# Kernel optimization log

Measured on AMD Instinct MI355X. Metric: run time of the kernel, lower is better.

Reference implementation:

```python
import jax, jax.numpy as jnp
import numpy as np

B, S, E = 2, 2048, 2048
KV, QPG, HD = 4, 4, 128  # 16 total heads, head_size=128
ROPE_THETA = 10000.0


def _rope_cos_sin(seq_len, head_size, dtype):
    inv_freq = 1.0 / (ROPE_THETA ** (jnp.arange(0, head_size, 2, dtype=jnp.float32) / head_size))
    pos = jnp.arange(seq_len, dtype=jnp.float32)
    freqs = pos[:, None] * inv_freq[None, :]            # [S, HD/2]
    emb = jnp.concatenate([freqs, freqs], axis=-1)       # [S, HD]
    return jnp.cos(emb).astype(dtype), jnp.sin(emb).astype(dtype)


def _rotate_half(x):
    x1, x2 = jnp.split(x, 2, axis=-1)
    return jnp.concatenate([-x2, x1], axis=-1)


def _apply_rope(x, cos, sin):
    # x: [..., S, HD]; cos/sin: [S, HD]
    return x * cos + _rotate_half(x) * sin


def setup_inputs() -> dict:
    key = jax.random.key(0)
    ks = jax.random.split(key, 8)
    scale = 0.02
    return {
        "x": jax.random.normal(ks[0], (B, S, E), jnp.float32),
        "wq": jax.random.normal(ks[1], (KV, QPG, HD, E), jnp.float32) * scale,
        "bq": jax.random.normal(ks[2], (KV, QPG, HD), jnp.float32) * scale,
        "wk": jax.random.normal(ks[3], (KV, HD, E), jnp.float32) * scale,
        "bk": jax.random.normal(ks[4], (KV, HD), jnp.float32) * scale,
        "wv": jax.random.normal(ks[5], (KV, HD, E), jnp.float32) * scale,
        "bv": jax.random.normal(ks[6], (KV, HD), jnp.float32) * scale,
        "wo": jax.random.normal(ks[7], (E, E), jnp.float32) * scale,
    }


def reference(x, wq, bq, wk, bk, wv, bv, wo):
    # QKV projections (out_first linear: y = W x + b)
    q = jnp.einsum('bse,kghe->bkgsh', x, wq) + bq[None, :, :, None, :]   # [B,KV,QPG,S,HD]
    k = jnp.einsum('bse,khe->bksh', x, wk) + bk[None, :, None, :]        # [B,KV,S,HD]
    v = jnp.einsum('bse,khe->bksh', x, wv) + bv[None, :, None, :]        # [B,KV,S,HD]

    cos, sin = _rope_cos_sin(S, HD, x.dtype)
    q = _apply_rope(q, cos, sin)
    k = _apply_rope(k, cos, sin)

    # GQA scaled dot-product attention with causal mask
    scale = 1.0 / jnp.sqrt(jnp.asarray(HD, x.dtype))
    scores = jnp.einsum('bkgsh,bkth->bkgst', q, k) * scale               # [B,KV,QPG,S,S]
    causal = jnp.tril(jnp.ones((S, S), dtype=bool))
    scores = jnp.where(causal, scores, jnp.asarray(-1e9, scores.dtype))
    att = jax.nn.softmax(scores, axis=-1)
    out = jnp.einsum('bkgst,bkth->bkgsh', att, v)                        # [B,KV,QPG,S,HD]

    # flatten (kv_heads, q_heads_per_group, head_size) -> heads*head_size and project
    out = out.transpose(0, 3, 1, 2, 4).reshape(B, S, KV * QPG * HD)      # [B,S,E]
    return jnp.einsum('bsf,ef->bse', out, wo)
```

## Files before the change

### kernel.cpp

```cpp
#include <hip/hip_runtime.h>

typedef unsigned short u16;
typedef short s16x8 __attribute__((ext_vector_type(8)));
typedef float f32x4 __attribute__((ext_vector_type(4)));
typedef float f32x16 __attribute__((ext_vector_type(16)));

__device__ __forceinline__ u16 f2bf(float f) {
  union { float f; unsigned u; } x; x.f = f;
  unsigned r = (x.u + 0x7fffu + ((x.u >> 16) & 1u)) >> 16;
  return (u16)r;
}
__device__ __forceinline__ unsigned bfbits_t(float f) {
  union { float f; unsigned u; } x; x.f = f;
  return x.u >> 16;
}
__device__ __forceinline__ float bf2f(u16 u) {
  union { unsigned u; float f; } x; x.u = ((unsigned)u) << 16;
  return x.f;
}

__device__ __forceinline__ void load_lds16(const u16* g, void* lds) {
  __builtin_amdgcn_global_load_lds(
      (const __attribute__((address_space(1))) unsigned int*)g,
      (__attribute__((address_space(3))) unsigned int*)lds, 16, 0, 0);
}

__global__ __launch_bounds__(256) void prep_kernel(
    const float* __restrict__ x,
    const float* __restrict__ wq, const float* __restrict__ wk,
    const float* __restrict__ wv,
    const float* __restrict__ bq, const float* __restrict__ bk,
    const float* __restrict__ bv,
    const float* __restrict__ wo,
    u16* __restrict__ xb, u16* __restrict__ wqkv,
    float* __restrict__ bqkv, u16* __restrict__ wob,
    float* __restrict__ cosb, float* __restrict__ sinb) {
  const int R0 = 2097152;
  const int R1 = R0 + 1572864;
  const int R2 = R1 + 1048576;
  const int R3 = R2 + 768;
  const int R4 = R3 + 131072;
  for (int id = blockIdx.x * 256 + threadIdx.x; id < R4; id += gridDim.x * 256) {
    if (id < R0) {
      float4 v = ((const float4*)x)[id];
      u16* d = xb + (size_t)id * 4;
      d[0] = f2bf(v.x); d[1] = f2bf(v.y); d[2] = f2bf(v.z); d[3] = f2bf(v.w);
    } else if (id < R1) {
      int g = id - R0;
      int row = g >> 9, c4 = (g & 511) * 4;
      const float* src; int srow;
      if (row < 2048)      { src = wq; srow = row; }
      else if (row < 2560) { src = wk; srow = row - 2048; }
      else                 { src = wv; srow = row - 2560; }
      float4 v = *(const float4*)&src[(size_t)srow * 2048 + c4];
      u16* d = wqkv + (size_t)row * 2048 + c4;
      d[0] = f2bf(v.x); d[1] = f2bf(v.y); d[2] = f2bf(v.z); d[3] = f2bf(v.w);
    } else if (id < R2) {
      int g = id - R1;
      float4 v = ((const float4*)wo)[g];
      u16* d = wob + (size_t)g * 4;
      d[0] = f2bf(v.x); d[1] = f2bf(v.y); d[2] = f2bf(v.z); d[3] = f2bf(v.w);
    } else if (id < R3) {
      int g4 = (id - R2) * 4;
      float4 v;
      if (g4 < 2048)      v = *(const float4*)&bq[g4];
      else if (g4 < 2560) v = *(const float4*)&bk[g4 - 2048];
      else                v = *(const float4*)&bv[g4 - 2560];
      *(float4*)&bqkv[g4] = v;
    } else {
      int g = id - R3;
      int s = g >> 6, i = g & 63;
      float freq = powf(10000.0f, -(float)i / 64.0f);
      float ang = (float)s * freq;
      cosb[g] = cosf(ang);
      sinb[g] = sinf(ang);
    }
  }
}

__global__ __launch_bounds__(256) void rope_all_kernel(u16* __restrict__ Qb,
                                                       u16* __restrict__ Kbuf,
                                                       const float* __restrict__ cosb,
                                                       const float* __restrict__ sinb) {
  const int total = (32 + 8) * 2048 * 64;
  for (int id = blockIdx.x * 256 + threadIdx.x; id < total; id += gridDim.x * 256) {
    int i = id & 63;
    int rs = id >> 6;
    int s = rs & 2047;
    u16* p;
    size_t base;
    if (rs < 65536) { p = Qb;   base = (size_t)rs * 128; }
    else            { p = Kbuf; base = (size_t)(rs - 65536) * 128; }
    float x1 = bf2f(p[base + i]);
    float x2 = bf2f(p[base + i + 64]);
    float c = cosb[s * 64 + i], sn = sinb[s * 64 + i];
    p[base + i]      = f2bf(x1 * c - x2 * sn);
    p[base + i + 64] = f2bf(x2 * c + x1 * sn);
  }
}

__global__ __launch_bounds__(256) void transpose_v_kernel(const u16* __restrict__ V,
                                                          u16* __restrict__ Vt) {
  __shared__ u16 tile[64][130];
  const int t = threadIdx.x;
  const int hb = blockIdx.x, s0 = blockIdx.y * 64;
  const u16* src = V + ((size_t)hb * 2048 + s0) * 128;
#pragma unroll
  for (int i = 0; i < 4; ++i) {
    int c = i * 256 + t;
    int s = c >> 4, d8 = (c & 15) * 8;
    *(s16x8*)&tile[s][d8] = *(const s16x8*)&src[(size_t)s * 128 + d8];
  }
  __syncthreads();
  u16* dst = Vt + (size_t)hb * 128 * 2048 + s0;
#pragma unroll
  for (int i = 0; i < 4; ++i) {
    int c = i * 256 + t;
    int d = c & 127, s8 = (c >> 7) * 8;
    s16x8 v;
#pragma unroll
    for (int e = 0; e < 8; ++e) v[e] = (short)tile[s8 + e][d];
    *(s16x8*)&dst[(size_t)d * 2048 + s8] = v;
  }
}

__global__ __launch_bounds__(512) void gemm_bt_kernel(
    const u16* __restrict__ A, const u16* __restrict__ Bw,
    const float* __restrict__ bias,
    float* __restrict__ C, int ldc,
    u16* __restrict__ Qp, u16* __restrict__ Kp, u16* __restrict__ Vp,
    int M, int N, int K, int mode) {
  __shared__ u16 sA[128 * 64];
  __shared__ u16 sB[128 * 64];
  const int t = threadIdx.x;
  const int w = t >> 6, l = t & 63;
  const int lg = l >> 4, lr = l & 15;
  const int wm = (w >> 2) * 64, wn = (w & 3) * 32;
  const int m0 = blockIdx.y * 128, n0 = blockIdx.x * 128;

  f32x4 acc[4][2];
#pragma unroll
  for (int i = 0; i < 4; ++i)
#pragma unroll
    for (int j = 0; j < 2; ++j)
#pragma unroll
      for (int r = 0; r < 4; ++r) acc[i][j][r] = 0.0f;

  for (int k0 = 0; k0 < K; k0 += 64) {
#pragma unroll
    for (int i = 0; i < 2; ++i) {
      int c = i * 512 + t;
      int row = c >> 3, cc = (c & 7) ^ (row & 7);
      load_lds16(A + (size_t)(m0 + row) * K + k0 + cc * 8,
                 (char*)sA + i * 8192 + w * 1024);
      load_lds16(Bw + (size_t)(n0 + row) * K + k0 + cc * 8,
                 (char*)sB + i * 8192 + w * 1024);
    }
    __syncthreads();
#pragma unroll
    for (int kc = 0; kc < 2; ++kc) {
      const int rch = (((kc * 4 + lg) ^ (lr & 7)) * 8);
      s16x8 af[4], bf[2];
#pragma unroll
      for (int m = 0; m < 4; ++m)
        af[m] = *(const s16x8*)&sA[(wm + m * 16 + lr) * 64 + rch];
#pragma unroll
      for (int n = 0; n < 2; ++n)
        bf[n] = *(const s16x8*)&sB[(wn + n * 16 + lr) * 64 + rch];
#pragma unroll
      for (int m = 0; m < 4; ++m)
#pragma unroll
        for (int n = 0; n < 2; ++n)
          acc[m][n] = __builtin_amdgcn_mfma_f32_16x16x32_bf16(af[m], bf[n], acc[m][n], 0, 0, 0);
    }
    __syncthreads();
  }

#pragma unroll
  for (int m = 0; m < 4; ++m) {
#pragma unroll
    for (int n = 0; n < 2; ++n) {
#pragma unroll
      for (int r = 0; r < 4; ++r) {
        int row = m0 + wm + m * 16 + (lg << 2) + r;
        int col = n0 + wn + n * 16 + lr;
        float val = acc[m][n][r];
        if (mode == 0) {
          val += bias[col];
          int b = row >> 11, s = row & 2047;
          u16 bvv = f2bf(val);
          if (col < 2048) {
            int h = col >> 7, d = col & 127;
            Qp[(((size_t)(b * 16 + h)) * 2048 + s) * 128 + d] = bvv;
          } else if (col < 2560) {
            int cc = col - 2048; int kh = cc >> 7, d = cc & 127;
            Kp[(((size_t)(b * 4 + kh)) * 2048 + s) * 128 + d] = bvv;
          } else {
            int cc = col - 2560; int kh = cc >> 7, d = cc & 127;
            Vp[(((size_t)(b * 4 + kh)) * 2048 + s) * 128 + d] = bvv;
          }
        } else {
          C[(size_t)row * ldc + col] = val;
        }
      }
    }
  }
}

__device__ const int PH_QC[16] = {7,-1, 7,0, 6,-1, 6,1, 5,-1, 5,2, 4,-1, 4,3};
__device__ const int PH_J0[16] = {0, 0, 18,0, 0, 0, 18,0, 0, 0, 18,0, 0, 0, 18,0};
__device__ const int PH_NT[16] = {18,0, 14,4, 18,0, 10,8, 18,0, 6,12, 18,0, 2,16};
__device__ const int PH_MD[16] = {1, 0, 2, 0, 1, 0, 2, 0, 1, 0, 2, 0, 1, 0, 2, 0};

__global__ __launch_bounds__(512) void flash_mfma_kernel(const u16* __restrict__ Q,
                                                         const u16* __restrict__ Kb,
                                                         const u16* __restrict__ Vtb,
                                                         u16* __restrict__ O,
                                                         u16* __restrict__ po,
                                                         float* __restrict__ pml) {
  const int S = 2048;
  __shared__ u16 sK[64 * 128];
  __shared__ u16 sVt[2 * 128 * 64];

  const int t = threadIdx.x, w = t >> 6, l = t & 63;
  const int l31 = l & 31, hi = l >> 5;
  const int bh = blockIdx.x, b = bh >> 4, h = bh & 15, kvh = h >> 2;
  const int slot = blockIdx.y;

  const u16* kbase = Kb + ((size_t)(b * 4 + kvh)) * S * 128;
  const u16* vtbase = Vtb + ((size_t)(b * 4 + kvh)) * 128 * S;

  const float C2 = 0.12753785f;

  auto stageK = [&](int kt) {
#pragma unroll
    for (int i = 0; i < 2; ++i) {
      int c = i * 512 + w * 64 + l;
      int j = c >> 4, cc = (c & 15) ^ (j & 7);
      load_lds16(kbase + ((size_t)(kt * 64 + j) * 128 + cc * 8),
                 (char*)sK + (i * 8192 + w * 1024));
    }
  };
  auto stageV = [&](int kt, int buf) {
#pragma unroll
    for (int i = 0; i < 2; ++i) {
      int c = i * 512 + w * 64 + l;
      int d = c >> 3, cc = (c & 7) ^ (d & 7);
      load_lds16(vtbase + ((size_t)d * S + kt * 64 + cc * 8),
                 (char*)sVt + buf * 16384 + (i * 8192 + w * 1024));
    }
  };

#pragma unroll 1
  for (int ph = 0; ph < 2; ++ph) {
    const int qc = PH_QC[slot * 2 + ph];
    const int ntc = PH_NT[slot * 2 + ph];
    if (ntc == 0) break;
    const int j0 = PH_J0[slot * 2 + ph];
    const int md = PH_MD[slot * 2 + ph];
    const int qw = qc * 256 + w * 32;
    const int q_glob = qw + l31;

    const u16* qbase = Q + ((size_t)bh * S + qw) * 128;
    s16x8 qb[8];
#pragma unroll
    for (int ks = 0; ks < 8; ++ks)
      qb[ks] = *(const s16x8*)&qbase[(size_t)l31 * 128 + ks * 16 + hi * 8];

    f32x16 o0, o1, o2, o3;
#pragma unroll
    for (int r = 0; r < 16; ++r) { o0[r] = 0.f; o1[r] = 0.f; o2[r] = 0.f; o3[r] = 0.f; }
    float mrun = -3e38f, lsum = 0.0f;

    stageV(j0, 0);
    stageK(j0);
    __syncthreads();

    int cur = 0;
    for (int kt2 = 0; kt2 < ntc; ++kt2) {
      const int kt = j0 + kt2;
      const bool act = (kt * 64 <= qw + 31);
      const bool more = (kt2 + 1 < ntc);

      if (more) stageV(kt + 1, cur ^ 1);

      f32x16 sc0, sc1;
      if (act) {
#pragma unroll
        for (int r = 0; r < 16; ++r) { sc0[r] = 0.f; sc1[r] = 0.f; }
        __builtin_amdgcn_s_setprio(1);
#pragma unroll
        for (int ks = 0; ks < 8; ++ks) {
          int chk = (2 * ks + hi) ^ (l31 & 7);
          s16x8 kf0 = *(const s16x8*)&sK[l31 * 128 + chk * 8];
          s16x8 kf1 = *(const s16x8*)&sK[(32 + l31) * 128 + chk * 8];
          sc0 = __builtin_amdgcn_mfma_f32_32x32x16_bf16(kf0, qb[ks], sc0, 0, 0, 0);
          sc1 = __builtin_amdgcn_mfma_f32_32x32x16_bf16(kf1, qb[ks], sc1, 0, 0, 0);
        }
        __builtin_amdgcn_s_setprio(0);
      }

      __syncthreads();

      if (more) stageK(kt + 1);

      if (act) {
        const u16* sVc = &sVt[cur * 8192];

        if (kt * 64 + 63 > qw) {
          const int j0m = kt * 64;
#pragma unroll
          for (int r = 0; r < 16; ++r) {
            int jr = j0m + (r & 3) + 8 * (r >> 2) + 4 * hi;
            sc0[r] = (jr <= q_glob) ? sc0[r] : -3e38f;
            sc1[r] = (jr + 32 <= q_glob) ? sc1[r] : -3e38f;
          }
        }

        float tm[16];
#pragma unroll
        for (int r = 0; r < 16; ++r) tm[r] = fmaxf(sc0[r], sc1[r]);
#pragma unroll
        for (int s2 = 8; s2 >= 1; s2 >>= 1)
#pragma unroll
          for (int r = 0; r < s2; ++r) tm[r] = fmaxf(tm[r], tm[r + s2]);
        float mt = fmaxf(tm[0], __shfl_xor(tm[0], 32));
        float mt2 = mt * C2;
        bool resc = (mt2 > mrun + 8.0f);
        if (resc) {
          float Mn = mt2;
          float corr = exp2f(mrun - Mn);
          lsum *= corr;
#pragma unroll
          for (int r = 0; r < 16; ++r) {
            o0[r] *= corr; o1[r] *= corr; o2[r] *= corr; o3[r] *= corr;
          }
          mrun = Mn;
        }
        const float Mn = mrun;

        unsigned pk[16];
        float lacc = 0.0f;
#pragma unroll
        for (int m = 0; m < 8; ++m) {
          float pa_ = exp2f(__builtin_fmaf(sc0[2 * m], C2, -Mn));
          float pb_ = exp2f(__builtin_fmaf(sc0[2 * m + 1], C2, -Mn));
          lacc += pa_ + pb_;
          pk[m] = (bfbits_t(pb_) << 16) | bfbits_t(pa_);
        }
#pragma unroll
        for (int m = 0; m < 8; ++m) {
          float pa_ = exp2f(__builtin_fmaf(sc1[2 * m], C2, -Mn));
          float pb_ = exp2f(__builtin_fmaf(sc1[2 * m + 1], C2, -Mn));
          lacc += pa_ + pb_;
          pk[8 + m] = (bfbits_t(pb_) << 16) | bfbits_t(pa_);
        }
        lsum += lacc;

        unsigned pkx[16];
#pragma unroll
        for (int i = 0; i < 16; ++i) pkx[i] = __shfl_xor(pk[i], 32);

        __builtin_amdgcn_s_setprio(1);
#pragma unroll
        for (int ks = 0; ks < 4; ++ks) {
          const int base = (ks >> 1) * 8 + 4 * (ks & 1);
          unsigned pw[4];
          pw[0] = hi ? pkx[base + 2] : pk[base + 0];
          pw[1] = hi ? pkx[base + 3] : pk[base + 1];
          pw[2] = hi ? pk[base + 2] : pkx[base + 0];
          pw[3] = hi ? pk[base + 3] : pkx[base + 1];
          s16x8 pa = *(const s16x8*)pw;
#pragma unroll
          for (int dt = 0; dt < 4; ++dt) {
            int d = dt * 32 + l31;
            s16x8 vt = *(const s16x8*)&sVc[d * 64 + (((2 * ks + hi) ^ (d & 7)) * 8)];
            if (dt == 0) o0 = __builtin_amdgcn_mfma_f32_32x32x16_bf16(vt, pa, o0, 0, 0, 0);
            if (dt == 1) o1 = __builtin_amdgcn_mfma_f32_32x32x16_bf16(vt, pa, o1, 0, 0, 0);
            if (dt == 2) o2 = __builtin_amdgcn_mfma_f32_32x32x16_bf16(vt, pa, o2, 0, 0, 0);
            if (dt == 3) o3 = __builtin_amdgcn_mfma_f32_32x32x16_bf16(vt, pa, o3, 0, 0, 0);
          }
        }
        __builtin_amdgcn_s_setprio(0);
      }

      __syncthreads();
      cur ^= 1;
    }

    float ls = lsum + __shfl_xor(lsum, 32);
    float inv = (ls > 0.0f) ? 1.0f / ls : 0.0f;
    if (md == 0) {
      size_t obase = ((size_t)b * S + q_glob) * 2048 + h * 128;
#pragma unroll
      for (int dt = 0; dt < 4; ++dt) {
        const f32x16& ov = (dt == 0) ? o0 : (dt == 1) ? o1 : (dt == 2) ? o2 : o3;
#pragma unroll
        for (int g = 0; g < 4; ++g) {
          int d0 = dt * 32 + 8 * g + 4 * hi;
          unsigned u0 = (unsigned)f2bf(ov[4 * g] * inv) | ((unsigned)f2bf(ov[4 * g + 1] * inv) << 16);
          unsigned u1 = (unsigned)f2bf(ov[4 * g + 2] * inv) | ((unsigned)f2bf(ov[4 * g + 3] * inv) << 16);
          uint2 u; u.x = u0; u.y = u1;
          *(uint2*)&O[obase + d0] = u;
        }
      }
    } else {
      const int pid = ((bh << 2) + (qc - 4)) * 2 + (md - 1);
      const int qrow = w * 32 + l31;
      size_t pbase = (size_t)pid * 32768 + (size_t)qrow * 128;
#pragma unroll
      for (int dt = 0; dt < 4; ++dt) {
        const f32x16& ov = (dt == 0) ? o0 : (dt == 1) ? o1 : (dt == 2) ? o2 : o3;
#pragma unroll
        for (int g = 0; g < 4; ++g) {
          int d0 = dt * 32 + 8 * g + 4 * hi;
          unsigned u0 = (unsigned)f2bf(ov[4 * g] * inv) | ((unsigned)f2bf(ov[4 * g + 1] * inv) << 16);
          unsigned u1 = (unsigned)f2bf(ov[4 * g + 2] * inv) | ((unsigned)f2bf(ov[4 * g + 3] * inv) << 16);
          uint2 u; u.x = u0; u.y = u1;
          *(uint2*)&po[pbase + d0] = u;
        }
      }
      if (hi == 0) {
        pml[pid * 512 + qrow * 2]     = mrun;
        pml[pid * 512 + qrow * 2 + 1] = ls;
      }
    }
    if (ph == 0 && PH_NT[slot * 2 + 1] != 0) __syncthreads();
  }
}

__global__ __launch_bounds__(256) void flash_merge_kernel(const u16* __restrict__ po,
                                                          const float* __restrict__ pml,
                                                          u16* __restrict__ att) {
  const int t = threadIdx.x;
  const int tl = blockIdx.x >> 4;
  const int row = (blockIdx.x & 15) * 16 + (t >> 4);
  const int d8 = (t & 15) * 8;
  const int hh2 = tl >> 2, qc = (tl & 3) + 4;
  const int pid0 = tl * 2, pid1 = pid0 + 1;
  float m0 = pml[pid0 * 512 + row * 2], l0 = pml[pid0 * 512 + row * 2 + 1];
  float m1 = pml[pid1 * 512 + row * 2], l1 = pml[pid1 * 512 + row * 2 + 1];
  float M = fmaxf(m0, m1);
  float w0 = l0 * exp2f(m0 - M), w1 = l1 * exp2f(m1 - M);
  float inv = 1.0f / (w0 + w1);
  w0 *= inv; w1 *= inv;
  s16x8 a = *(const s16x8*)&po[(size_t)pid0 * 32768 + row * 128 + d8];
  s16x8 c = *(const s16x8*)&po[(size_t)pid1 * 32768 + row * 128 + d8];
  int b = hh2 >> 4, hh = hh2 & 15;
  size_t base = ((size_t)b * 2048 + qc * 256 + row) * 2048 + hh * 128 + d8;
  u16 outv[8];
#pragma unroll
  for (int e = 0; e < 8; ++e)
    outv[e] = f2bf(w0 * bf2f((u16)a[e]) + w1 * bf2f((u16)c[e]));
  *(s16x8*)&att[base] = *(const s16x8*)outv;
}


extern "C" void kernel_launch(void* const* d_in, const int* in_sizes, int n_in,
                              void* d_out, int out_size, void* d_ws, size_t ws_size,
                              hipStream_t stream) {
  const float* x  = (const float*)d_in[0];
  const float* wq = (const float*)d_in[1];
  const float* bq = (const float*)d_in[2];
  const float* wk = (const float*)d_in[3];
  const float* bk = (const float*)d_in[4];
  const float* wv = (const float*)d_in[5];
  const float* bv = (const float*)d_in[6];
  const float* wo = (const float*)d_in[7];
  float* out = (float*)d_out;

  char* ws = (char*)d_ws;
  u16* xb    = (u16*)ws;    ws += (size_t)4096 * 2048 * 2;
  u16* wqkv  = (u16*)ws;    ws += (size_t)3072 * 2048 * 2;
  float* bqkv = (float*)ws; ws += (size_t)3072 * 4;
  u16* wob   = (u16*)ws;    ws += (size_t)2048 * 2048 * 2;
  u16* Qb    = (u16*)ws;    ws += (size_t)32 * 2048 * 128 * 2;
  u16* Kbuf  = (u16*)ws;    ws += (size_t)8 * 2048 * 128 * 2;
  u16* Vbuf  = (u16*)ws;    ws += (size_t)8 * 2048 * 128 * 2;
  u16* Vt    = (u16*)ws;    ws += (size_t)8 * 128 * 2048 * 2;
  float* cosb = (float*)ws; ws += (size_t)2048 * 64 * 4;
  float* sinb = (float*)ws; ws += (size_t)2048 * 64 * 4;
  u16* att   = (u16*)ws;    ws += (size_t)4096 * 2048 * 2;

  u16* po = xb;
  float* pml = (float*)Vbuf;

  prep_kernel<<<2048, 256, 0, stream>>>(x, wq, wk, wv, bq, bk, bv, wo,
                                        xb, wqkv, bqkv, wob, cosb, sinb);

  gemm_bt_kernel<<<dim3(24, 32), 512, 0, stream>>>(xb, wqkv, bqkv, nullptr, 0,
                                                   Qb, Kbuf, Vbuf, 4096, 3072, 2048, 0);
  transpose_v_kernel<<<dim3(8, 32), 256, 0, stream>>>(Vbuf, Vt);
  rope_all_kernel<<<2048, 256, 0, stream>>>(Qb, Kbuf, cosb, sinb);

  flash_mfma_kernel<<<dim3(32, 8), 512, 0, stream>>>(Qb, Kbuf, Vt, att, po, pml);
  flash_merge_kernel<<<2048, 256, 0, stream>>>(po, pml, att);

  gemm_bt_kernel<<<dim3(16, 32), 512, 0, stream>>>(att, wob, nullptr, out, 2048,
                                                   nullptr, nullptr, nullptr, 4096, 2048, 2048, 1);
}
```

Measured before the change: 198.1 us.

## Double attention KV tile from 64 to 128 keys per iteration

Widens the flash-attention key/value tile from 64 to 128 rows, doubling the shared-memory buffers, changing the swizzle to 16-chunk XOR, and computing four score tiles per step with two P·V sub-blocks. The phase tables are halved to match the new tile count. This halves the number of loop iterations and __syncthreads barriers and amortizes softmax max/rescale work over more keys. In exchange it raises LDS use (about 96KB per block) and register pressure, and puts more masked work on the causal diagonal.

```diff
diff --git a/kernel.cpp b/kernel.cpp
--- a/kernel.cpp
+++ b/kernel.cpp
@@ -208,9 +208,9 @@
 }
 
 __device__ const int PH_QC[16] = {7,-1, 7,0, 6,-1, 6,1, 5,-1, 5,2, 4,-1, 4,3};
-__device__ const int PH_J0[16] = {0, 0, 18,0, 0, 0, 18,0, 0, 0, 18,0, 0, 0, 18,0};
-__device__ const int PH_NT[16] = {18,0, 14,4, 18,0, 10,8, 18,0, 6,12, 18,0, 2,16};
-__device__ const int PH_MD[16] = {1, 0, 2, 0, 1, 0, 2, 0, 1, 0, 2, 0, 1, 0, 2, 0};
+__device__ const int PH_J0[16] = {0,0, 9,0, 0,0, 9,0, 0,0, 9,0, 0,0, 9,0};
+__device__ const int PH_NT[16] = {9,0, 7,2, 9,0, 5,4, 9,0, 3,6, 9,0, 1,8};
+__device__ const int PH_MD[16] = {1,0, 2,0, 1,0, 2,0, 1,0, 2,0, 1,0, 2,0};
 
 __global__ __launch_bounds__(512) void flash_mfma_kernel(const u16* __restrict__ Q,
                                                          const u16* __restrict__ Kb,
@@ -219,8 +219,8 @@
                                                          u16* __restrict__ po,
                                                          float* __restrict__ pml) {
   const int S = 2048;
-  __shared__ u16 sK[64 * 128];
-  __shared__ u16 sVt[2 * 128 * 64];
+  __shared__ u16 sK[128 * 128];
+  __shared__ u16 sVt[2 * 128 * 128];
 
   const int t = threadIdx.x, w = t >> 6, l = t & 63;
   const int l31 = l & 31, hi = l >> 5;
@@ -234,20 +234,20 @@
 
   auto stageK = [&](int kt) {
 #pragma unroll
-    for (int i = 0; i < 2; ++i) {
-      int c = i * 512 + w * 64 + l;
-      int j = c >> 4, cc = (c & 15) ^ (j & 7);
-      load_lds16(kbase + ((size_t)(kt * 64 + j) * 128 + cc * 8),
+    for (int i = 0; i < 4; ++i) {
+      int c = i * 512 + t;
+      int j = c >> 4, cc = (c & 15) ^ (j & 15);
+      load_lds16(kbase + ((size_t)(kt * 128 + j) * 128 + cc * 8),
                  (char*)sK + (i * 8192 + w * 1024));
     }
   };
   auto stageV = [&](int kt, int buf) {
 #pragma unroll
-    for (int i = 0; i < 2; ++i) {
-      int c = i * 512 + w * 64 + l;
-      int d = c >> 3, cc = (c & 7) ^ (d & 7);
-      load_lds16(vtbase + ((size_t)d * S + kt * 64 + cc * 8),
-                 (char*)sVt + buf * 16384 + (i * 8192 + w * 1024));
+    for (int i = 0; i < 4; ++i) {
+      int c = i * 512 + t;
+      int d = c >> 4, cc = (c & 15) ^ (d & 15);
+      load_lds16(vtbase + ((size_t)d * S + kt * 128 + cc * 8),
+                 (char*)sVt + buf * 32768 + (i * 8192 + w * 1024));
     }
   };
 
@@ -279,23 +279,28 @@
     int cur = 0;
     for (int kt2 = 0; kt2 < ntc; ++kt2) {
       const int kt = j0 + kt2;
-      const bool act = (kt * 64 <= qw + 31);
+      const bool act = (kt * 128 <= qw + 31);
       const bool more = (kt2 + 1 < ntc);
 
       if (more) stageV(kt + 1, cur ^ 1);
 
-      f32x16 sc0, sc1;
+      f32x16 sc0, sc1, sc2, sc3;
       if (act) {
 #pragma unroll
-        for (int r = 0; r < 16; ++r) { sc0[r] = 0.f; sc1[r] = 0.f; }
+        for (int r = 0; r < 16; ++r) { sc0[r] = 0.f; sc1[r] = 0.f; sc2[r] = 0.f; sc3[r] = 0.f; }
+        const int chkb = (l31 & 15);
         __builtin_amdgcn_s_setprio(1);
 #pragma unroll
         for (int ks = 0; ks < 8; ++ks) {
-          int chk = (2 * ks + hi) ^ (l31 & 7);
-          s16x8 kf0 = *(const s16x8*)&sK[l31 * 128 + chk * 8];
-          s16x8 kf1 = *(const s16x8*)&sK[(32 + l31) * 128 + chk * 8];
+          int chk = ((2 * ks + hi) ^ chkb) * 8;
+          s16x8 kf0 = *(const s16x8*)&sK[(l31) * 128 + chk];
+          s16x8 kf1 = *(const s16x8*)&sK[(32 + l31) * 128 + chk];
+          s16x8 kf2 = *(const s16x8*)&sK[(64 + l31) * 128 + chk];
+          s16x8 kf3 = *(const s16x8*)&sK[(96 + l31) * 128 + chk];
           sc0 = __builtin_amdgcn_mfma_f32_32x32x16_bf16(kf0, qb[ks], sc0, 0, 0, 0);
           sc1 = __builtin_amdgcn_mfma_f32_32x32x16_bf16(kf1, qb[ks], sc1, 0, 0, 0);
+          sc2 = __builtin_amdgcn_mfma_f32_32x32x16_bf16(kf2, qb[ks], sc2, 0, 0, 0);
+          sc3 = __builtin_amdgcn_mfma_f32_32x32x16_bf16(kf3, qb[ks], sc3, 0, 0, 0);
         }
         __builtin_amdgcn_s_setprio(0);
       }
@@ -305,21 +310,24 @@
       if (more) stageK(kt + 1);
 
       if (act) {
-        const u16* sVc = &sVt[cur * 8192];
-
-        if (kt * 64 + 63 > qw) {
-          const int j0m = kt * 64;
+        const u16* sVc = &sVt[cur * 16384];
+
+        if (kt * 128 + 127 > qw) {
+          const int j0m = kt * 128;
 #pragma unroll
           for (int r = 0; r < 16; ++r) {
             int jr = j0m + (r & 3) + 8 * (r >> 2) + 4 * hi;
             sc0[r] = (jr <= q_glob) ? sc0[r] : -3e38f;
             sc1[r] = (jr + 32 <= q_glob) ? sc1[r] : -3e38f;
+            sc2[r] = (jr + 64 <= q_glob) ? sc2[r] : -3e38f;
+            sc3[r] = (jr + 96 <= q_glob) ? sc3[r] : -3e38f;
           }
         }
 
         float tm[16];
 #pragma unroll
-        for (int r = 0; r < 16; ++r) tm[r] = fmaxf(sc0[r], sc1[r]);
+        for (int r = 0; r < 16; ++r)
+          tm[r] = fmaxf(fmaxf(sc0[r], sc1[r]), fmaxf(sc2[r], sc3[r]));
 #pragma unroll
         for (int s2 = 8; s2 >= 1; s2 >>= 1)
 #pragma unroll
@@ -338,50 +346,92 @@
           mrun = Mn;
         }
         const float Mn = mrun;
-
-        unsigned pk[16];
         float lacc = 0.0f;
-#pragma unroll
-        for (int m = 0; m < 8; ++m) {
-          float pa_ = exp2f(__builtin_fmaf(sc0[2 * m], C2, -Mn));
-          float pb_ = exp2f(__builtin_fmaf(sc0[2 * m + 1], C2, -Mn));
-          lacc += pa_ + pb_;
-          pk[m] = (bfbits_t(pb_) << 16) | bfbits_t(pa_);
-        }
-#pragma unroll
-        for (int m = 0; m < 8; ++m) {
-          float pa_ = exp2f(__builtin_fmaf(sc1[2 * m], C2, -Mn));
-          float pb_ = exp2f(__builtin_fmaf(sc1[2 * m + 1], C2, -Mn));
-          lacc += pa_ + pb_;
-          pk[8 + m] = (bfbits_t(pb_) << 16) | bfbits_t(pa_);
+
+        {
+          unsigned pk[16];
+#pragma unroll
+          for (int m = 0; m < 8; ++m) {
+            float pa_ = exp2f(__builtin_fmaf(sc0[2 * m], C2, -Mn));
+            float pb_ = exp2f(__builtin_fmaf(sc0[2 * m + 1], C2, -Mn));
+            lacc += pa_ + pb_;
+            pk[m] = (bfbits_t(pb_) << 16) | bfbits_t(pa_);
+          }
+#pragma unroll
+          for (int m = 0; m < 8; ++m) {
+            float pa_ = exp2f(__builtin_fmaf(sc1[2 * m], C2, -Mn));
+            float pb_ = exp2f(__builtin_fmaf(sc1[2 * m + 1], C2, -Mn));
+            lacc += pa_ + pb_;
+            pk[8 + m] = (bfbits_t(pb_) << 16) | bfbits_t(pa_);
+          }
+          unsigned pkx[16];
+#pragma unroll
+          for (int i = 0; i < 16; ++i) pkx[i] = __shfl_xor(pk[i], 32);
+          __builtin_amdgcn_s_setprio(1);
+#pragma unroll
+          for (int ks = 0; ks < 4; ++ks) {
+            const int base = (ks >> 1) * 8 + 4 * (ks & 1);
+            unsigned pw[4];
+            pw[0] = hi ? pkx[base + 2] : pk[base + 0];
+            pw[1] = hi ? pkx[base + 3] : pk[base + 1];
+            pw[2] = hi ? pk[base + 2] : pkx[base + 0];
+            pw[3] = hi ? pk[base + 3] : pkx[base + 1];
+            s16x8 pa = *(const s16x8*)pw;
+#pragma unroll
+            for (int dt = 0; dt < 4; ++dt) {
+              int d = dt * 32 + l31;
+              s16x8 vt = *(const s16x8*)&sVc[d * 128 + (((2 * ks + hi) ^ (d & 15)) * 8)];
+              if (dt == 0) o0 = __builtin_amdgcn_mfma_f32_32x32x16_bf16(vt, pa, o0, 0, 0, 0);
+              if (dt == 1) o1 = __builtin_amdgcn_mfma_f32_32x32x16_bf16(vt, pa, o1, 0, 0, 0);
+              if (dt == 2) o2 = __builtin_amdgcn_mfma_f32_32x32x16_bf16(vt, pa, o2, 0, 0, 0);
+              if (dt == 3) o3 = __builtin_amdgcn_mfma_f32_32x32x16_bf16(vt, pa, o3, 0, 0, 0);
+            }
+          }
+          __builtin_amdgcn_s_setprio(0);
+        }
+
+        {
+          unsigned pk[16];
+#pragma unroll
+          for (int m = 0; m < 8; ++m) {
+            float pa_ = exp2f(__builtin_fmaf(sc2[2 * m], C2, -Mn));
+            float pb_ = exp2f(__builtin_fmaf(sc2[2 * m + 1], C2, -Mn));
+            lacc += pa_ + pb_;
+            pk[m] = (bfbits_t(pb_) << 16) | bfbits_t(pa_);
+          }
+#pragma unroll
+          for (int m = 0; m < 8; ++m) {
+            float pa_ = exp2f(__builtin_fmaf(sc3[2 * m], C2, -Mn));
+            float pb_ = exp2f(__builtin_fmaf(sc3[2 * m + 1], C2, -Mn));
+            lacc += pa_ + pb_;
+            pk[8 + m] = (bfbits_t(pb_) << 16) | bfbits_t(pa_);
+          }
+          unsigned pkx[16];
+#pragma unroll
+          for (int i = 0; i < 16; ++i) pkx[i] = __shfl_xor(pk[i], 32);
+          __builtin_amdgcn_s_setprio(1);
+#pragma unroll
+          for (int ks = 0; ks < 4; ++ks) {
+            const int base = (ks >> 1) * 8 + 4 * (ks & 1);
+            unsigned pw[4];
+            pw[0] = hi ? pkx[base + 2] : pk[base + 0];
+            pw[1] = hi ? pkx[base + 3] : pk[base + 1];
+            pw[2] = hi ? pk[base + 2] : pkx[base + 0];
+            pw[3] = hi ? pk[base + 3] : pkx[base + 1];
+            s16x8 pa = *(const s16x8*)pw;
+#pragma unroll
+            for (int dt = 0; dt < 4; ++dt) {
+              int d = dt * 32 + l31;
+              s16x8 vt = *(const s16x8*)&sVc[d * 128 + (((8 + 2 * ks + hi) ^ (d & 15)) * 8)];
+              if (dt == 0) o0 = __builtin_amdgcn_mfma_f32_32x32x16_bf16(vt, pa, o0, 0, 0, 0);
+              if (dt == 1) o1 = __builtin_amdgcn_mfma_f32_32x32x16_bf16(vt, pa, o1, 0, 0, 0);
+              if (dt == 2) o2 = __builtin_amdgcn_mfma_f32_32x32x16_bf16(vt, pa, o2, 0, 0, 0);
+              if (dt == 3) o3 = __builtin_amdgcn_mfma_f32_32x32x16_bf16(vt, pa, o3, 0, 0, 0);
+            }
+          }
+          __builtin_amdgcn_s_setprio(0);
         }
         lsum += lacc;
-
-        unsigned pkx[16];
-#pragma unroll
-        for (int i = 0; i < 16; ++i) pkx[i] = __shfl_xor(pk[i], 32);
-
-        __builtin_amdgcn_s_setprio(1);
-#pragma unroll
-        for (int ks = 0; ks < 4; ++ks) {
-          const int base = (ks >> 1) * 8 + 4 * (ks & 1);
-          unsigned pw[4];
-          pw[0] = hi ? pkx[base + 2] : pk[base + 0];
-          pw[1] = hi ? pkx[base + 3] : pk[base + 1];
-          pw[2] = hi ? pk[base + 2] : pkx[base + 0];
-          pw[3] = hi ? pk[base + 3] : pkx[base + 1];
-          s16x8 pa = *(const s16x8*)pw;
-#pragma unroll
-          for (int dt = 0; dt < 4; ++dt) {
-            int d = dt * 32 + l31;
-            s16x8 vt = *(const s16x8*)&sVc[d * 64 + (((2 * ks + hi) ^ (d & 7)) * 8)];
-            if (dt == 0) o0 = __builtin_amdgcn_mfma_f32_32x32x16_bf16(vt, pa, o0, 0, 0, 0);
-            if (dt == 1) o1 = __builtin_amdgcn_mfma_f32_32x32x16_bf16(vt, pa, o1, 0, 0, 0);
-            if (dt == 2) o2 = __builtin_amdgcn_mfma_f32_32x32x16_bf16(vt, pa, o2, 0, 0, 0);
-            if (dt == 3) o3 = __builtin_amdgcn_mfma_f32_32x32x16_bf16(vt, pa, o3, 0, 0, 0);
-          }
-        }
-        __builtin_amdgcn_s_setprio(0);
       }
 
       __syncthreads();
```

Result: no change. 197.6 us, median of 5 (-0.2%).
